# Optimization experiments

Measured on AMD Instinct MI355X. Metric: run time of the kernel, lower is better.

## Reference

```python
import jax, jax.numpy as jnp
import numpy as np

NEG_SLOPE = 0.2  # PyG GATConv default


def _gat_layer(h_in, W, a_src, a_dst, b, src, dst, n_nodes, heads, out_dim):
    """One GATConv layer (PyG semantics: messages flow src -> dst,
    softmax over incoming edges of each dst node)."""
    h = (h_in @ W).reshape(n_nodes, heads, out_dim)          # [N,H,C]
    alpha_s = jnp.sum(h * a_src, axis=-1)                    # [N,H]
    alpha_d = jnp.sum(h * a_dst, axis=-1)                    # [N,H]
    e = jax.nn.leaky_relu(alpha_s[src] + alpha_d[dst], NEG_SLOPE)  # [E,H]
    # segment softmax over dst groups (numerically stable)
    m = jax.ops.segment_max(e, dst, num_segments=n_nodes)    # [N,H]
    ex = jnp.exp(e - m[dst])                                 # [E,H]
    s = jax.ops.segment_sum(ex, dst, num_segments=n_nodes)   # [N,H]
    alpha = ex / (s[dst] + 1e-16)                            # [E,H]
    msg = h[src] * alpha[:, :, None]                         # [E,H,C]
    out = jax.ops.segment_sum(msg, dst, num_segments=n_nodes)  # [N,H,C]
    return out.reshape(n_nodes, heads * out_dim) + b


def setup_inputs() -> dict:
    N, E = 50000, 800000
    IN, HID, H = 128, 64, 4
    key = jax.random.key(0)
    ks = jax.random.split(key, 10)
    x = jax.random.normal(ks[0], (N, IN), dtype=jnp.float32)
    edge_index = jax.random.randint(ks[1], (2, E), 0, N, dtype=jnp.int64)
    sc = 0.05
    return {
        "x": x,
        "edge_index": edge_index,
        "W1": jax.random.normal(ks[2], (IN, H * HID), dtype=jnp.float32) * sc,
        "att_src1": jax.random.normal(ks[3], (H, HID), dtype=jnp.float32) * sc,
        "att_dst1": jax.random.normal(ks[4], (H, HID), dtype=jnp.float32) * sc,
        "b1": jnp.zeros((H * HID,), dtype=jnp.float32),
        "W2": jax.random.normal(ks[5], (H * HID, HID), dtype=jnp.float32) * sc,
        "att_src2": jax.random.normal(ks[6], (1, HID), dtype=jnp.float32) * sc,
        "att_dst2": jax.random.normal(ks[7], (1, HID), dtype=jnp.float32) * sc,
        "b2": jnp.zeros((HID,), dtype=jnp.float32),
    }


def reference(x, edge_index, W1, att_src1, att_dst1, b1, W2, att_src2, att_dst2, b2):
    N = x.shape[0]
    H, HID = att_src1.shape
    # add self loops (PyG GATConv default add_self_loops=True)
    loops = jnp.arange(N, dtype=edge_index.dtype)
    src = jnp.concatenate([edge_index[0], loops])
    dst = jnp.concatenate([edge_index[1], loops])
    h = _gat_layer(x, W1, att_src1, att_dst1, b1, src, dst, N, H, HID)
    h = jax.nn.relu(h)
    out = _gat_layer(h, W2, att_src2, att_dst2, b2, src, dst, N, 1, HID)
    return out
```

## Files before the change

### kernel.cpp

```cpp
#include <hip/hip_runtime.h>
#include <cstdint>

#define LRELU_SLOPE 0.2f

typedef short bf16x8_t __attribute__((ext_vector_type(8)));
typedef float f32x4_t  __attribute__((ext_vector_type(4)));

__device__ __forceinline__ float bf2f(unsigned int u) { return __uint_as_float(u << 16); }
__device__ __forceinline__ unsigned short f2bf(float f) {
    unsigned int x = __float_as_uint(f);
    return (unsigned short)((x + 0x7fffu + ((x >> 16) & 1u)) >> 16);
}

struct PrepDesc { const void* ssrc[6]; float* sdst[6]; int slen[6]; };
__global__ __launch_bounds__(256) void prep_k(const unsigned short* __restrict__ xh,
                                              const int* __restrict__ ei32,
                                              const void* __restrict__ w1raw,
                                              const void* __restrict__ w2raw,
                                              unsigned short* __restrict__ Wt1,
                                              unsigned short* __restrict__ Wt2,
                                              PrepDesc d, int* __restrict__ flags,
                                              int* __restrict__ offs, int N) {
    __shared__ int s_ei, s_cnt;
    if (threadIdx.x == 0) { s_ei = 0; s_cnt = 0; }
    __syncthreads();
    const int t = threadIdx.x;
    int e_or = 0;
#pragma unroll
    for (int j = 0; j < 4; j++) if (ei32[2 * (t * 4 + j) + 1] != 0) e_or = 1;
    if (e_or) atomicOr(&s_ei, 1);
    int c = 0;
#pragma unroll
    for (int j = 0; j < 8; j++) {
        unsigned short h = xh[t * 8 + j];
        int e = (h >> 7) & 0xFF;
        if (e >= 117 && e < 134) c++;
    }
    atomicAdd(&s_cnt, c);
    __syncthreads();
    const int isb = (s_cnt >= 1600) ? 1 : 0;
    const int i32 = s_ei;
    if (blockIdx.x == 0 && t == 0) { flags[0] = i32; flags[1] = isb; }
    const int gstride = gridDim.x * blockDim.x;
    const int gid = blockIdx.x * blockDim.x + t;
    for (int i = gid; i < 128 * 256; i += gstride) {
        int k = i >> 8, n = i & 255;
        unsigned short b = isb ? ((const unsigned short*)w1raw)[i] : f2bf(((const float*)w1raw)[i]);
        Wt1[n * 128 + k] = b;
    }
    for (int i = gid; i < 256 * 64; i += gstride) {
        int k = i >> 6, n = i & 63;
        unsigned short b = isb ? ((const unsigned short*)w2raw)[i] : f2bf(((const float*)w2raw)[i]);
        Wt2[n * 256 + k] = b;
    }
#pragma unroll
    for (int s = 0; s < 6; s++)
        for (int i = gid; i < d.slen[s]; i += gstride) {
            float v = isb ? bf2f((unsigned int)((const unsigned short*)d.ssrc[s])[i])
                          : ((const float*)d.ssrc[s])[i];
            d.sdst[s][i] = v;
        }
    for (int i = gid; i <= N; i += gstride) offs[i] = 0;
}

__global__ __launch_bounds__(256) void gemm1_k(const void* __restrict__ xraw,
                                               const unsigned short* __restrict__ Wt,
                                               const float* __restrict__ asw_,
                                               const float* __restrict__ adw_,
                                               unsigned short* __restrict__ h,
                                               float* __restrict__ as_, float* __restrict__ ad_,
                                               int M, const int* __restrict__ flags) {
    __shared__ unsigned short xs[64 * 136];
    const int tid = threadIdx.x;
    const long row0 = (long)blockIdx.x * 64;
    if (flags[1] != 0) {
        const uint4* xv = (const uint4*)xraw;
        const long base = row0 * 16;
        const long lim = (long)M * 16 - base;
#pragma unroll
        for (int i = 0; i < 4; i++) {
            int idx = tid + i * 256;
            uint4 v;
            if (idx < lim) v = xv[base + idx];
            else { v.x = v.y = v.z = v.w = 0u; }
            int r = idx >> 4, c8 = idx & 15;
            *(uint4*)&xs[r * 136 + c8 * 8] = v;
        }
    } else {
        const float4* xv = (const float4*)xraw;
        const long base = row0 * 32;
        const long lim = (long)M * 32 - base;
#pragma unroll
        for (int i = 0; i < 8; i++) {
            int idx = tid + i * 256;
            float4 v;
            if (idx < lim) v = xv[base + idx];
            else { v.x = v.y = v.z = v.w = 0.f; }
            int r = idx >> 5, c4 = idx & 31;
            ushort4 o;
            o.x = f2bf(v.x); o.y = f2bf(v.y); o.z = f2bf(v.z); o.w = f2bf(v.w);
            *(ushort4*)&xs[r * 136 + c4 * 4] = o;
        }
    }
    __syncthreads();
    const int wv = tid >> 6;
    const int lane = tid & 63;
    const int l16 = lane & 15, quad = lane >> 4;
    bf16x8_t af[4];
#pragma unroll
    for (int ks = 0; ks < 4; ks++)
        af[ks] = *(const bf16x8_t*)&xs[(wv * 16 + l16) * 136 + ks * 32 + quad * 8];
    float psA[4] = {0.f, 0.f, 0.f, 0.f}, pdA[4] = {0.f, 0.f, 0.f, 0.f};
#pragma unroll
    for (int t = 0; t < 16; t++) {
        f32x4_t acc = {0.f, 0.f, 0.f, 0.f};
#pragma unroll
        for (int ks = 0; ks < 4; ks++) {
            bf16x8_t bf = *(const bf16x8_t*)(Wt + (size_t)(t * 16 + l16) * 128 + ks * 32 + quad * 8);
            acc = __builtin_amdgcn_mfma_f32_16x16x32_bf16(af[ks], bf, acc, 0, 0, 0);
        }
        const float aswv = asw_[t * 16 + l16];
        const float adwv = adw_[t * 16 + l16];
#pragma unroll
        for (int r = 0; r < 4; r++) {
            long grow = row0 + wv * 16 + quad * 4 + r;
            if (grow < M) h[grow * 256 + t * 16 + l16] = f2bf(acc[r]);
            psA[r] = fmaf(acc[r], aswv, psA[r]);
            pdA[r] = fmaf(acc[r], adwv, pdA[r]);
        }
        if ((t & 3) == 3) {
            const int hd = t >> 2;
#pragma unroll
            for (int r = 0; r < 4; r++) {
                float ps = psA[r], pd = pdA[r];
#pragma unroll
                for (int o = 8; o > 0; o >>= 1) {
                    ps += __shfl_down(ps, o, 16);
                    pd += __shfl_down(pd, o, 16);
                }
                long grow = row0 + wv * 16 + quad * 4 + r;
                if (l16 == 0 && grow < M) { as_[grow * 4 + hd] = ps; ad_[grow * 4 + hd] = pd; }
                psA[r] = 0.f; pdA[r] = 0.f;
            }
        }
    }
}

__global__ __launch_bounds__(256) void gemm2_k(const unsigned short* __restrict__ x,
                                               const unsigned short* __restrict__ Wt,
                                               const float* __restrict__ asw_,
                                               const float* __restrict__ adw_,
                                               unsigned short* __restrict__ h,
                                               float* __restrict__ as_, float* __restrict__ ad_,
                                               int M) {
    __shared__ unsigned short xs[64 * 264];
    const int tid = threadIdx.x;
    const long row0 = (long)blockIdx.x * 64;
    const uint4* xv = (const uint4*)x;
    const long base = row0 * 32;
    const long lim = (long)M * 32 - base;
#pragma unroll
    for (int i = 0; i < 8; i++) {
        int idx = tid + i * 256;
        uint4 v;
        if (idx < lim) v = xv[base + idx];
        else { v.x = v.y = v.z = v.w = 0u; }
        int r = idx >> 5, c8 = idx & 31;
        *(uint4*)&xs[r * 264 + c8 * 8] = v;
    }
    __syncthreads();
    const int wv = tid >> 6;
    const int lane = tid & 63;
    const int l16 = lane & 15, quad = lane >> 4;
    bf16x8_t af[8];
#pragma unroll
    for (int ks = 0; ks < 8; ks++)
        af[ks] = *(const bf16x8_t*)&xs[(wv * 16 + l16) * 264 + ks * 32 + quad * 8];
    float psA[4] = {0.f, 0.f, 0.f, 0.f}, pdA[4] = {0.f, 0.f, 0.f, 0.f};
#pragma unroll
    for (int t = 0; t < 4; t++) {
        f32x4_t acc = {0.f, 0.f, 0.f, 0.f};
#pragma unroll
        for (int ks = 0; ks < 8; ks++) {
            bf16x8_t bf = *(const bf16x8_t*)(Wt + (size_t)(t * 16 + l16) * 256 + ks * 32 + quad * 8);
            acc = __builtin_amdgcn_mfma_f32_16x16x32_bf16(af[ks], bf, acc, 0, 0, 0);
        }
        const float aswv = asw_[t * 16 + l16];
        const float adwv = adw_[t * 16 + l16];
#pragma unroll
        for (int r = 0; r < 4; r++) {
            long grow = row0 + wv * 16 + quad * 4 + r;
            if (grow < M) h[grow * 64 + t * 16 + l16] = f2bf(acc[r]);
            psA[r] = fmaf(acc[r], aswv, psA[r]);
            pdA[r] = fmaf(acc[r], adwv, pdA[r]);
        }
    }
#pragma unroll
    for (int r = 0; r < 4; r++) {
        float ps = psA[r], pd = pdA[r];
#pragma unroll
        for (int o = 8; o > 0; o >>= 1) { ps += __shfl_down(ps, o, 16); pd += __shfl_down(pd, o, 16); }
        long grow = row0 + wv * 16 + quad * 4 + r;
        if (l16 == 0 && grow < M) { as_[grow] = ps; ad_[grow] = pd; }
    }
}

__global__ void hist_k(const int* __restrict__ ei, int E, int N,
                       const int* __restrict__ flags, int* __restrict__ deg) {
    int i = blockIdx.x * blockDim.x + threadIdx.x;
    int T = E + N;
    if (i >= T) return;
    int is64 = (flags[0] == 0);
    int d;
    if (i < E) { long k = (long)E + i; d = is64 ? ei[2 * k] : ei[k]; }
    else d = i - E;
    if ((unsigned)d < (unsigned)N) atomicAdd(&deg[d], 1);
}

__global__ __launch_bounds__(1024) void scan1_k(int* __restrict__ offs, int* __restrict__ bsum, int N) {
    __shared__ int tmp[2][1024];
    const int tid = threadIdx.x;
    const int i = blockIdx.x * 1024 + tid;
    int v = (i < N) ? offs[i] : 0;
    tmp[0][tid] = v;
    __syncthreads();
    int val = v, pb = 0;
    for (int off = 1; off < 1024; off <<= 1) {
        int t = (tid >= off) ? tmp[pb][tid - off] : 0;
        tmp[pb ^ 1][tid] = val + t;
        val += t;
        __syncthreads();
        pb ^= 1;
    }
    if (i < N) offs[i] = val - v;
    if (tid == 1023) bsum[blockIdx.x] = val;
}

__global__ __launch_bounds__(1024) void scan2_k(int* __restrict__ bsum, int NB) {
    __shared__ int tmp[2][1024];
    const int tid = threadIdx.x;
    int v = (tid < NB) ? bsum[tid] : 0;
    tmp[0][tid] = v;
    __syncthreads();
    int val = v, pb = 0;
    for (int off = 1; off < 1024; off <<= 1) {
        int t = (tid >= off) ? tmp[pb][tid - off] : 0;
        tmp[pb ^ 1][tid] = val + t;
        val += t;
        __syncthreads();
        pb ^= 1;
    }
    if (tid < NB) bsum[tid] = val - v;
}

__global__ __launch_bounds__(1024) void scan3_k(int* __restrict__ offs, int* __restrict__ cursor,
                                                const int* __restrict__ bsum, int N, int T) {
    const int i = blockIdx.x * 1024 + threadIdx.x;
    if (i < N) { int o = offs[i] + bsum[blockIdx.x]; offs[i] = o; cursor[i] = o; }
    if (i == 0) offs[N] = T;
}

__global__ void scat_p_k(const int* __restrict__ ei, int E, int N,
                         const int* __restrict__ flags, int* __restrict__ cursor,
                         int* __restrict__ esrc, float4* __restrict__ pw,
                         const float* __restrict__ as1, const float* __restrict__ ad1) {
    int i = blockIdx.x * blockDim.x + threadIdx.x;
    int T = E + N;
    if (i >= T) return;
    int is64 = (flags[0] == 0);
    int s, d;
    if (i < E) {
        s = is64 ? ei[2 * (long)i] : ei[i];
        long k = (long)E + i;
        d = is64 ? ei[2 * k] : ei[k];
    } else { s = d = i - E; }
    if ((unsigned)d >= (unsigned)N) return;
    if ((unsigned)s >= (unsigned)N) s = 0;
    int pos = atomicAdd(&cursor[d], 1);
    esrc[pos] = s;
    float4 a = ((const float4*)as1)[s];
    float4 b = ((const float4*)ad1)[d];
    float e0 = a.x + b.x, e1 = a.y + b.y, e2 = a.z + b.z, e3 = a.w + b.w;
    e0 = e0 > 0.f ? e0 : LRELU_SLOPE * e0;
    e1 = e1 > 0.f ? e1 : LRELU_SLOPE * e1;
    e2 = e2 > 0.f ? e2 : LRELU_SLOPE * e2;
    e3 = e3 > 0.f ? e3 : LRELU_SLOPE * e3;
    float4 p; p.x = __expf(e0); p.y = __expf(e1); p.z = __expf(e2); p.w = __expf(e3);
    pw[pos] = p;
}

__global__ __launch_bounds__(256) void agg1_k(const uint2* __restrict__ hfeat,
                                              const int* __restrict__ offs,
                                              const int* __restrict__ esrc,
                                              const float4* __restrict__ pw,
                                              const float* __restrict__ bias,
                                              unsigned short* __restrict__ outb, int N) {
    const int wid = threadIdx.x >> 6, lane = threadIdx.x & 63;
    const long node = (long)blockIdx.x * 4 + wid;
    if (node >= N) return;
    const int hh = lane >> 4;
    const bool lo = hh < 2, evn = (hh & 1) == 0;
    float a0 = 0.f, a1 = 0.f, a2 = 0.f, a3 = 0.f, s = 0.f;
    const int beg = __builtin_amdgcn_readfirstlane(offs[node]);
    const int end = __builtin_amdgcn_readfirstlane(offs[node + 1]);
    int j = beg;
#define P_SEL(P) (lo ? (evn ? P.x : P.y) : (evn ? P.z : P.w))
#define EDGE(v, p) { \
        float f0 = bf2f(v.x & 0xffffu), f1 = bf2f(v.x >> 16); \
        float f2 = bf2f(v.y & 0xffffu), f3 = bf2f(v.y >> 16); \
        a0 = fmaf(p, f0, a0); a1 = fmaf(p, f1, a1); \
        a2 = fmaf(p, f2, a2); a3 = fmaf(p, f3, a3); s += p; }
    for (; j + 8 <= end; j += 8) {
        int si[8];
#pragma unroll
        for (int u = 0; u < 8; u++) si[u] = esrc[j + u];
        uint2 vv[8];
#pragma unroll
        for (int u = 0; u < 8; u++) vv[u] = hfeat[(long)si[u] * 64 + lane];
        float4 PP[8];
#pragma unroll
        for (int u = 0; u < 8; u++) PP[u] = pw[j + u];
#pragma unroll
        for (int u = 0; u < 8; u++) { const float p = P_SEL(PP[u]); EDGE(vv[u], p) }
    }
    for (; j < end; j++) {
        const int s0 = esrc[j];
        const uint2 v0 = hfeat[(long)s0 * 64 + lane];
        const float4 P0 = pw[j];
        const float p0 = P_SEL(P0);
        EDGE(v0, p0)
    }
#undef EDGE
    const float4 bi = ((const float4*)bias)[lane];
    const float inv = 1.f / s;
    uint2 o;
    o.x = (unsigned)f2bf(fmaxf(fmaf(a0, inv, bi.x), 0.f)) |
          ((unsigned)f2bf(fmaxf(fmaf(a1, inv, bi.y), 0.f)) << 16);
    o.y = (unsigned)f2bf(fmaxf(fmaf(a2, inv, bi.z), 0.f)) |
          ((unsigned)f2bf(fmaxf(fmaf(a3, inv, bi.w), 0.f)) << 16);
    ((uint2*)outb)[node * 64 + lane] = o;
}

__global__ __launch_bounds__(256) void agg2_k(const unsigned short* __restrict__ hfeat,
                                              const float* __restrict__ as_,
                                              const float* __restrict__ ad_,
                                              const int* __restrict__ offs,
                                              const int* __restrict__ esrc,
                                              const float* __restrict__ bias,
                                              unsigned short* __restrict__ outb,
                                              float* __restrict__ outf,
                                              const int* __restrict__ flags, int N) {
    const int wid = threadIdx.x >> 6, lane = threadIdx.x & 63;
    const long node = (long)blockIdx.x * 4 + wid;
    if (node >= N) return;
    const float adn = ad_[node];
    float s = 0.f, acc = 0.f;
    const int beg = __builtin_amdgcn_readfirstlane(offs[node]);
    const int end = __builtin_amdgcn_readfirstlane(offs[node + 1]);
    int j = beg;
#define LRELU(e) ((e) > 0.f ? (e) : LRELU_SLOPE * (e))
    for (; j + 8 <= end; j += 8) {
        int si[8];
#pragma unroll
        for (int u = 0; u < 8; u++) si[u] = esrc[j + u];
        float hv[8];
#pragma unroll
        for (int u = 0; u < 8; u++) hv[u] = bf2f((unsigned int)hfeat[(long)si[u] * 64 + lane]);
        float av[8];
#pragma unroll
        for (int u = 0; u < 8; u++) av[u] = as_[si[u]];
#pragma unroll
        for (int u = 0; u < 8; u++) {
            const float p = __expf(LRELU(av[u] + adn));
            acc = fmaf(p, hv[u], acc); s += p;
        }
    }
    for (; j < end; j++) {
        const int s0 = esrc[j];
        const float h0 = bf2f((unsigned int)hfeat[(long)s0 * 64 + lane]);
        const float p0 = __expf(LRELU(as_[s0] + adn));
        acc = fmaf(p0, h0, acc); s += p0;
    }
#undef LRELU
    float v = acc / s + bias[lane];
    long o = node * 64 + lane;
    if (flags[1] != 0) outb[o] = f2bf(v);
    else               outf[o] = v;
}

static inline size_t alignup(size_t v, size_t a) { return (v + a - 1) & ~(a - 1); }

extern "C" void kernel_launch(void* const* d_in, const int* in_sizes, int n_in,
                              void* d_out, int out_size, void* d_ws, size_t ws_size,
                              hipStream_t stream) {
    const void* x  = d_in[0];
    const int*  ei = (const int*)d_in[1];

    const int N = in_sizes[0] / 128;
    const int E = in_sizes[1] / 2;
    const int T = E + N;
    const int NB = (N + 1023) / 1024;

    size_t off = 0;
    char* w = (char*)d_ws;
    auto take = [&](size_t bytes) { void* p = w + off; off = alignup(off + bytes, 256); return p; };

    int*   flags = (int*)take(256);
    unsigned short* Wt1 = (unsigned short*)take((size_t)256 * 128 * 2);
    unsigned short* Wt2 = (unsigned short*)take((size_t)64 * 256 * 2);
    float* as1w = (float*)take(256 * 4);
    float* ad1w = (float*)take(256 * 4);
    float* b1f  = (float*)take(256 * 4);
    float* as2w = (float*)take(64 * 4);
    float* ad2w = (float*)take(64 * 4);
    float* b2f  = (float*)take(64 * 4);
    unsigned short* h1b   = (unsigned short*)take((size_t)N * 256 * 2);
    unsigned short* act1b = (unsigned short*)take((size_t)N * 256 * 2);
    float* as1 = (float*)take((size_t)N * 4 * 4);
    float* ad1 = (float*)take((size_t)N * 4 * 4);
    float* as2 = (float*)take((size_t)N * 4);
    float* ad2 = (float*)take((size_t)N * 4);
    int* offs   = (int*)take((size_t)(N + 1) * 4);
    int* cursor = (int*)take((size_t)N * 4);
    int* bsum   = (int*)take(1024 * 4);
    int* esrc   = (int*)take((size_t)T * 4);
    float4* pw  = (float4*)take((size_t)T * 16);
    unsigned short* h2b = h1b;

    PrepDesc pd;
    pd.ssrc[0] = d_in[3]; pd.sdst[0] = as1w; pd.slen[0] = 256;
    pd.ssrc[1] = d_in[4]; pd.sdst[1] = ad1w; pd.slen[1] = 256;
    pd.ssrc[2] = d_in[5]; pd.sdst[2] = b1f;  pd.slen[2] = 256;
    pd.ssrc[3] = d_in[7]; pd.sdst[3] = as2w; pd.slen[3] = 64;
    pd.ssrc[4] = d_in[8]; pd.sdst[4] = ad2w; pd.slen[4] = 64;
    pd.ssrc[5] = d_in[9]; pd.sdst[5] = b2f;  pd.slen[5] = 64;
    prep_k<<<64, 256, 0, stream>>>((const unsigned short*)x, ei, d_in[2], d_in[6],
                                   Wt1, Wt2, pd, flags, offs, N);

    hist_k<<<(T + 255) / 256, 256, 0, stream>>>(ei, E, N, flags, offs);
    gemm1_k<<<(N + 63) / 64, 256, 0, stream>>>(x, Wt1, as1w, ad1w, h1b, as1, ad1, N, flags);
    scan1_k<<<NB, 1024, 0, stream>>>(offs, bsum, N);
    scan2_k<<<1, 1024, 0, stream>>>(bsum, NB);
    scan3_k<<<NB, 1024, 0, stream>>>(offs, cursor, bsum, N, T);
    scat_p_k<<<(T + 255) / 256, 256, 0, stream>>>(ei, E, N, flags, cursor, esrc, pw, as1, ad1);
    agg1_k<<<(N + 3) / 4, 256, 0, stream>>>((const uint2*)h1b, offs, esrc, pw, b1f, act1b, N);
    gemm2_k<<<(N + 63) / 64, 256, 0, stream>>>(act1b, Wt2, as2w, ad2w, h2b, as2, ad2, N);
    agg2_k<<<(N + 3) / 4, 256, 0, stream>>>(h2b, as2, ad2, offs, esrc, b2f,
                                            (unsigned short*)d_out, (float*)d_out, flags, N);
}
```

Measured before the change: 336.7 us.

## Fuse three-pass scan into one kernel and recompute edge weights in aggregation

The three-kernel prefix scan (block scan, block-sum scan, add-back) becomes a single kernel. Each block publishes its sum with a flag, and a wave spins on the flags of all blocks to form its carry. The per-edge exp weights are no longer computed in the scatter kernel and stored as a float4 array. agg1 now recomputes them from the per-node attention scalars, which removes writing and reading 16 bytes per edge. The costs are an extra gather of as_ per edge and redundant exp work, and the spin-wait assumes every scan block (about 49) is resident at once.

```diff
diff --git a/kernel.cpp b/kernel.cpp
--- a/kernel.cpp
+++ b/kernel.cpp
@@ -20,7 +20,8 @@
                                               unsigned short* __restrict__ Wt1,
                                               unsigned short* __restrict__ Wt2,
                                               PrepDesc d, int* __restrict__ flags,
-                                              int* __restrict__ offs, int N) {
+                                              int* __restrict__ offs,
+                                              int* __restrict__ bflag, int N) {
     __shared__ int s_ei, s_cnt;
     if (threadIdx.x == 0) { s_ei = 0; s_cnt = 0; }
     __syncthreads();
@@ -39,8 +40,7 @@
     atomicAdd(&s_cnt, c);
     __syncthreads();
     const int isb = (s_cnt >= 1600) ? 1 : 0;
-    const int i32 = s_ei;
-    if (blockIdx.x == 0 && t == 0) { flags[0] = i32; flags[1] = isb; }
+    if (blockIdx.x == 0 && t == 0) { flags[0] = s_ei; flags[1] = isb; }
     const int gstride = gridDim.x * blockDim.x;
     const int gid = blockIdx.x * blockDim.x + t;
     for (int i = gid; i < 128 * 256; i += gstride) {
@@ -61,6 +61,7 @@
             d.sdst[s][i] = v;
         }
     for (int i = gid; i <= N; i += gstride) offs[i] = 0;
+    for (int i = gid; i < 1024; i += gstride) bflag[i] = 0;
 }
 
 __global__ __launch_bounds__(256) void gemm1_k(const void* __restrict__ xraw,
@@ -217,10 +218,14 @@
     if ((unsigned)d < (unsigned)N) atomicAdd(&deg[d], 1);
 }
 
-__global__ __launch_bounds__(1024) void scan1_k(int* __restrict__ offs, int* __restrict__ bsum, int N) {
+__global__ __launch_bounds__(1024) void scan_k(int* __restrict__ offs, int* __restrict__ cursor,
+                                               int* __restrict__ bsum, int* __restrict__ bflag,
+                                               int N, int T, int NB) {
     __shared__ int tmp[2][1024];
+    __shared__ int carry_s;
     const int tid = threadIdx.x;
-    const int i = blockIdx.x * 1024 + tid;
+    const int b = blockIdx.x;
+    const int i = b * 1024 + tid;
     int v = (i < N) ? offs[i] : 0;
     tmp[0][tid] = v;
     __syncthreads();
@@ -232,38 +237,37 @@
         __syncthreads();
         pb ^= 1;
     }
-    if (i < N) offs[i] = val - v;
-    if (tid == 1023) bsum[blockIdx.x] = val;
-}
-
-__global__ __launch_bounds__(1024) void scan2_k(int* __restrict__ bsum, int NB) {
-    __shared__ int tmp[2][1024];
-    const int tid = threadIdx.x;
-    int v = (tid < NB) ? bsum[tid] : 0;
-    tmp[0][tid] = v;
-    __syncthreads();
-    int val = v, pb = 0;
-    for (int off = 1; off < 1024; off <<= 1) {
-        int t = (tid >= off) ? tmp[pb][tid - off] : 0;
-        tmp[pb ^ 1][tid] = val + t;
-        val += t;
-        __syncthreads();
-        pb ^= 1;
-    }
-    if (tid < NB) bsum[tid] = val - v;
-}
-
-__global__ __launch_bounds__(1024) void scan3_k(int* __restrict__ offs, int* __restrict__ cursor,
-                                                const int* __restrict__ bsum, int N, int T) {
-    const int i = blockIdx.x * 1024 + threadIdx.x;
-    if (i < N) { int o = offs[i] + bsum[blockIdx.x]; offs[i] = o; cursor[i] = o; }
-    if (i == 0) offs[N] = T;
-}
-
-__global__ void scat_p_k(const int* __restrict__ ei, int E, int N,
-                         const int* __restrict__ flags, int* __restrict__ cursor,
-                         int* __restrict__ esrc, float4* __restrict__ pw,
-                         const float* __restrict__ as1, const float* __restrict__ ad1) {
+    const int lexcl = val - v;
+    if (tid == 1023) {
+        bsum[b] = val;
+        __threadfence();
+        atomicExch(&bflag[b], 1);
+    }
+    if (tid < 64) {
+        int myv = 0;
+        if (tid < NB) {
+            while (atomicAdd(&bflag[tid], 0) == 0) {}
+            myv = atomicAdd(&bsum[tid], 0);
+        }
+        int incl = myv;
+#pragma unroll
+        for (int o = 1; o < 64; o <<= 1) {
+            int t = __shfl_up(incl, o, 64);
+            if (tid >= o) incl += t;
+        }
+        int carry = (b == 0) ? 0 : __shfl(incl, b - 1, 64);
+        if (tid == 0) {
+            carry_s = carry;
+            if (b == 0) offs[N] = T;
+        }
+    }
+    __syncthreads();
+    if (i < N) { int o = lexcl + carry_s; offs[i] = o; cursor[i] = o; }
+}
+
+__global__ void scat_k(const int* __restrict__ ei, int E, int N,
+                       const int* __restrict__ flags, int* __restrict__ cursor,
+                       int* __restrict__ esrc) {
     int i = blockIdx.x * blockDim.x + threadIdx.x;
     int T = E + N;
     if (i >= T) return;
@@ -278,33 +282,25 @@
     if ((unsigned)s >= (unsigned)N) s = 0;
     int pos = atomicAdd(&cursor[d], 1);
     esrc[pos] = s;
-    float4 a = ((const float4*)as1)[s];
-    float4 b = ((const float4*)ad1)[d];
-    float e0 = a.x + b.x, e1 = a.y + b.y, e2 = a.z + b.z, e3 = a.w + b.w;
-    e0 = e0 > 0.f ? e0 : LRELU_SLOPE * e0;
-    e1 = e1 > 0.f ? e1 : LRELU_SLOPE * e1;
-    e2 = e2 > 0.f ? e2 : LRELU_SLOPE * e2;
-    e3 = e3 > 0.f ? e3 : LRELU_SLOPE * e3;
-    float4 p; p.x = __expf(e0); p.y = __expf(e1); p.z = __expf(e2); p.w = __expf(e3);
-    pw[pos] = p;
 }
 
 __global__ __launch_bounds__(256) void agg1_k(const uint2* __restrict__ hfeat,
                                               const int* __restrict__ offs,
                                               const int* __restrict__ esrc,
-                                              const float4* __restrict__ pw,
+                                              const float* __restrict__ as_,
+                                              const float* __restrict__ ad_,
                                               const float* __restrict__ bias,
                                               unsigned short* __restrict__ outb, int N) {
     const int wid = threadIdx.x >> 6, lane = threadIdx.x & 63;
     const long node = (long)blockIdx.x * 4 + wid;
     if (node >= N) return;
     const int hh = lane >> 4;
-    const bool lo = hh < 2, evn = (hh & 1) == 0;
+    const float adn = ad_[node * 4 + hh];
     float a0 = 0.f, a1 = 0.f, a2 = 0.f, a3 = 0.f, s = 0.f;
     const int beg = __builtin_amdgcn_readfirstlane(offs[node]);
     const int end = __builtin_amdgcn_readfirstlane(offs[node + 1]);
     int j = beg;
-#define P_SEL(P) (lo ? (evn ? P.x : P.y) : (evn ? P.z : P.w))
+#define LRELU(e) ((e) > 0.f ? (e) : LRELU_SLOPE * (e))
 #define EDGE(v, p) { \
         float f0 = bf2f(v.x & 0xffffu), f1 = bf2f(v.x >> 16); \
         float f2 = bf2f(v.y & 0xffffu), f3 = bf2f(v.y >> 16); \
@@ -317,17 +313,19 @@
         uint2 vv[8];
 #pragma unroll
         for (int u = 0; u < 8; u++) vv[u] = hfeat[(long)si[u] * 64 + lane];
-        float4 PP[8];
-#pragma unroll
-        for (int u = 0; u < 8; u++) PP[u] = pw[j + u];
-#pragma unroll
-        for (int u = 0; u < 8; u++) { const float p = P_SEL(PP[u]); EDGE(vv[u], p) }
+        float av[8];
+#pragma unroll
+        for (int u = 0; u < 8; u++) av[u] = as_[si[u] * 4 + hh];
+#pragma unroll
+        for (int u = 0; u < 8; u++) {
+            const float p = __expf(LRELU(av[u] + adn));
+            EDGE(vv[u], p)
+        }
     }
     for (; j < end; j++) {
         const int s0 = esrc[j];
         const uint2 v0 = hfeat[(long)s0 * 64 + lane];
-        const float4 P0 = pw[j];
-        const float p0 = P_SEL(P0);
+        const float p0 = __expf(LRELU(as_[s0 * 4 + hh] + adn));
         EDGE(v0, p0)
     }
 #undef EDGE
@@ -423,8 +421,8 @@
     int* offs   = (int*)take((size_t)(N + 1) * 4);
     int* cursor = (int*)take((size_t)N * 4);
     int* bsum   = (int*)take(1024 * 4);
+    int* bflag  = (int*)take(1024 * 4);
     int* esrc   = (int*)take((size_t)T * 4);
-    float4* pw  = (float4*)take((size_t)T * 16);
     unsigned short* h2b = h1b;
 
     PrepDesc pd;
@@ -435,15 +433,13 @@
     pd.ssrc[4] = d_in[8]; pd.sdst[4] = ad2w; pd.slen[4] = 64;
     pd.ssrc[5] = d_in[9]; pd.sdst[5] = b2f;  pd.slen[5] = 64;
     prep_k<<<64, 256, 0, stream>>>((const unsigned short*)x, ei, d_in[2], d_in[6],
-                                   Wt1, Wt2, pd, flags, offs, N);
+                                   Wt1, Wt2, pd, flags, offs, bflag, N);
 
     hist_k<<<(T + 255) / 256, 256, 0, stream>>>(ei, E, N, flags, offs);
     gemm1_k<<<(N + 63) / 64, 256, 0, stream>>>(x, Wt1, as1w, ad1w, h1b, as1, ad1, N, flags);
-    scan1_k<<<NB, 1024, 0, stream>>>(offs, bsum, N);
-    scan2_k<<<1, 1024, 0, stream>>>(bsum, NB);
-    scan3_k<<<NB, 1024, 0, stream>>>(offs, cursor, bsum, N, T);
-    scat_p_k<<<(T + 255) / 256, 256, 0, stream>>>(ei, E, N, flags, cursor, esrc, pw, as1, ad1);
-    agg1_k<<<(N + 3) / 4, 256, 0, stream>>>((const uint2*)h1b, offs, esrc, pw, b1f, act1b, N);
+    scan_k<<<NB, 1024, 0, stream>>>(offs, cursor, bsum, bflag, N, T, NB);
+    scat_k<<<(T + 255) / 256, 256, 0, stream>>>(ei, E, N, flags, cursor, esrc);
+    agg1_k<<<(N + 3) / 4, 256, 0, stream>>>((const uint2*)h1b, offs, esrc, as1, ad1, b1f, act1b, N);
     gemm2_k<<<(N + 63) / 64, 256, 0, stream>>>(act1b, Wt2, as2w, ad2w, h2b, as2, ad2, N);
     agg2_k<<<(N + 3) / 4, 256, 0, stream>>>(h2b, as2, ad2, offs, esrc, b2f,
                                             (unsigned short*)d_out, (float*)d_out, flags, N);
```

New measurement: 346.7 us. 1.03x slower.
